# Optimization experiments

Hardware: AMD Instinct MI355X
Metric: run time of the kernel (lower is better)

## Reference

```python
import jax, jax.numpy as jnp
import numpy as np

N = 100000
E = 1600000
NFEAT = 256
NHID = 64
NHEADS = 4
NCLASS = 32
ALPHA = 0.2  # LeakyReLU negative slope


def _xavier_normal(key, shape, gain=1.414):
    fan_in, fan_out = shape[-2], shape[-1]
    std = gain * np.sqrt(2.0 / (fan_in + fan_out))
    return (jax.random.normal(key, shape, jnp.float32) * std).astype(jnp.float32)


def setup_inputs() -> dict:
    key = jax.random.key(0)
    k = jax.random.split(key, 8)
    x = jax.random.normal(k[0], (N, NFEAT), jnp.float32)
    src = jax.random.randint(k[1], (E,), 0, N, jnp.int32)
    dst = jax.random.randint(k[2], (E,), 0, N, jnp.int32)
    # self-loops on the first N edges so every row has nonzero attention mass
    loop = jnp.arange(N, dtype=jnp.int32)
    src = src.at[:N].set(loop)
    dst = dst.at[:N].set(loop)
    edge_index = jnp.stack([src, dst])  # [2, E]
    W_heads = _xavier_normal(k[3], (NHEADS, NFEAT, NHID))
    # torch inits a as (1, 2*out): xavier fans are (2*out, 1)
    a_std = 1.414 * np.sqrt(2.0 / (2 * NHID + 1))
    a_heads = (jax.random.normal(k[4], (NHEADS, 2 * NHID), jnp.float32) * a_std)
    W_out = _xavier_normal(k[5], (NHEADS * NHID, NCLASS))
    a_out_std = 1.414 * np.sqrt(2.0 / (2 * NCLASS + 1))
    a_out = (jax.random.normal(k[6], (2 * NCLASS,), jnp.float32) * a_out_std)
    return {"x": x, "edge_index": edge_index, "W_heads": W_heads,
            "a_heads": a_heads, "W_out": W_out, "a_out": a_out}


def _gat_layer(x, W, a, src, dst):
    """One sparse GAT attention layer (dropout = identity, eval mode)."""
    h = x @ W                      # [N, O]
    O = W.shape[1]
    s_src = h @ a[:O]              # [N]
    s_dst = h @ a[O:]              # [N]
    # e_ij = exp(-leakyrelu(a . [h_i ; h_j])) for edge (i=src, j=dst)
    e = jnp.exp(-jax.nn.leaky_relu(s_src[src] + s_dst[dst], ALPHA))  # [E]
    rowsum = jax.ops.segment_sum(e, src, num_segments=N)             # [N]
    agg = jax.ops.segment_sum(e[:, None] * h[dst], src, num_segments=N)  # [N, O]
    return agg / rowsum[:, None]


def reference(x, edge_index, W_heads, a_heads, W_out, a_out):
    src, dst = edge_index[0], edge_index[1]
    # multi-head hidden layer (concat=True -> elu per head)
    heads = jax.vmap(lambda W, a: _gat_layer(x, W, a, src, dst))(W_heads, a_heads)  # [H, N, NHID]
    x1 = jax.nn.elu(heads).transpose(1, 0, 2).reshape(N, NHEADS * NHID)
    # output attention layer (concat=False), then elu + log_softmax in SpGAT.forward
    h2 = _gat_layer(x1, W_out, a_out, src, dst)  # [N, NCLASS]
    return jax.nn.log_softmax(jax.nn.elu(h2), axis=1)
```

## Files before the change

kernel.cpp:

```cpp
#include <hip/hip_runtime.h>
#include <cstdint>
#include <cstddef>

#define ALPHA 0.2f

__device__ __forceinline__ float lrelu(float x) { return x > 0.f ? x : ALPHA * x; }

__device__ __forceinline__ float qbf(float x)
{
    uint32_t u = __float_as_uint(x);
    uint32_t r = (u + 0x7FFFu + ((u >> 16) & 1u)) & 0xFFFF0000u;
    return __uint_as_float(r);
}

__global__ __launch_bounds__(256) void k_gemm1(const float* __restrict__ x,
                                               const float* __restrict__ Wh,
                                               float* __restrict__ H, int n)
{
    __shared__ float As[32][68];
    __shared__ float Bs[32][256];
    const int tid = threadIdx.x;
    const int row0 = blockIdx.x * 64;
    const int tx = tid & 15, ty = tid >> 4;

    float acc[4][16];
#pragma unroll
    for (int r = 0; r < 4; ++r)
#pragma unroll
        for (int c = 0; c < 16; ++c) acc[r][c] = 0.f;

    for (int k0 = 0; k0 < 256; k0 += 32) {
        for (int j = tid; j < 512; j += 256) {
            int r = j >> 3, kk = (j & 7) << 2;
            int gr = row0 + r; if (gr >= n) gr = n - 1;
            const float4 v = *(const float4*)&x[(size_t)gr * 256 + k0 + kk];
            As[kk + 0][r] = qbf(v.x); As[kk + 1][r] = qbf(v.y);
            As[kk + 2][r] = qbf(v.z); As[kk + 3][r] = qbf(v.w);
        }
        for (int j = tid; j < 2048; j += 256) {
            int kk = j >> 6, c4 = j & 63;
            int h = c4 >> 4, o = (c4 & 15) << 2;
            const float4 v = *(const float4*)&Wh[h * 16384 + (k0 + kk) * 64 + o];
            float* bp = &Bs[kk][c4 << 2];
            bp[0] = qbf(v.x); bp[1] = qbf(v.y); bp[2] = qbf(v.z); bp[3] = qbf(v.w);
        }
        __syncthreads();
#pragma unroll
        for (int kk = 0; kk < 32; ++kk) {
            const float4 a  = *(const float4*)&As[kk][ty << 2];
            const float4 b0 = *(const float4*)&Bs[kk][tx * 16 + 0];
            const float4 b1 = *(const float4*)&Bs[kk][tx * 16 + 4];
            const float4 b2 = *(const float4*)&Bs[kk][tx * 16 + 8];
            const float4 b3 = *(const float4*)&Bs[kk][tx * 16 + 12];
            const float av[4]  = {a.x, a.y, a.z, a.w};
            const float bv[16] = {b0.x, b0.y, b0.z, b0.w, b1.x, b1.y, b1.z, b1.w,
                                  b2.x, b2.y, b2.z, b2.w, b3.x, b3.y, b3.z, b3.w};
#pragma unroll
            for (int r = 0; r < 4; ++r)
#pragma unroll
                for (int c = 0; c < 16; ++c) acc[r][c] += av[r] * bv[c];
        }
        __syncthreads();
    }
#pragma unroll
    for (int r = 0; r < 4; ++r) {
        int gr = row0 + (ty << 2) + r;
        if (gr < n) {
            float* dst = &H[(size_t)gr * 256 + tx * 16];
#pragma unroll
            for (int i = 0; i < 4; ++i)
                *(float4*)&dst[4 * i] = make_float4(acc[r][4 * i + 0], acc[r][4 * i + 1],
                                                    acc[r][4 * i + 2], acc[r][4 * i + 3]);
        }
    }
}

__global__ __launch_bounds__(256) void k_scores1(const float* __restrict__ H,
                                                 const float* __restrict__ a,
                                                 float* __restrict__ s1src,
                                                 float* __restrict__ s1dst, int n)
{
    int gtid = blockIdx.x * 256 + threadIdx.x;
    int node = gtid >> 6, lane = gtid & 63;
    if (node >= n) return;
    int h = lane >> 4, o0 = (lane & 15) << 2;
    const float4 hv = *(const float4*)&H[(size_t)node * 256 + lane * 4];
    float as0 = qbf(a[h * 128 + o0 + 0]), as1 = qbf(a[h * 128 + o0 + 1]);
    float as2 = qbf(a[h * 128 + o0 + 2]), as3 = qbf(a[h * 128 + o0 + 3]);
    float ad0 = qbf(a[h * 128 + 64 + o0 + 0]), ad1 = qbf(a[h * 128 + 64 + o0 + 1]);
    float ad2 = qbf(a[h * 128 + 64 + o0 + 2]), ad3 = qbf(a[h * 128 + 64 + o0 + 3]);
    float ps = hv.x * as0 + hv.y * as1 + hv.z * as2 + hv.w * as3;
    float pd = hv.x * ad0 + hv.y * ad1 + hv.z * ad2 + hv.w * ad3;
#pragma unroll
    for (int m = 8; m >= 1; m >>= 1) {
        ps += __shfl_xor(ps, m);
        pd += __shfl_xor(pd, m);
    }
    if ((lane & 15) == 0) {
        s1src[node * 4 + h] = ps;
        s1dst[node * 4 + h] = pd;
    }
}

__global__ void k_zero(int* __restrict__ p, int n)
{
    int i = blockIdx.x * 256 + threadIdx.x;
    if (i < n) p[i] = 0;
}

__global__ void k_hist(const int* __restrict__ src, int* __restrict__ counts, int e)
{
    int i = blockIdx.x * 256 + threadIdx.x;
    if (i < e) atomicAdd(&counts[src[i]], 1);
}

__global__ __launch_bounds__(256) void k_blocksum(const int* __restrict__ counts,
                                                  int* __restrict__ bsum, int n)
{
    int tid = threadIdx.x;
    int i0 = blockIdx.x * 2048 + tid * 8;
    int s = 0;
#pragma unroll
    for (int k = 0; k < 8; ++k) {
        int i = i0 + k;
        if (i < n) s += counts[i];
    }
#pragma unroll
    for (int m = 32; m >= 1; m >>= 1) s += __shfl_xor(s, m);
    __shared__ int ws[4];
    int lane = tid & 63, wv = tid >> 6;
    if (lane == 0) ws[wv] = s;
    __syncthreads();
    if (tid == 0) bsum[blockIdx.x] = ws[0] + ws[1] + ws[2] + ws[3];
}

__global__ void k_scanmeta(const int* __restrict__ bsum, int* __restrict__ choff, int nchunk)
{
    int lane = threadIdx.x;
    int v = (lane < nchunk) ? bsum[lane] : 0;
    int incl = v;
#pragma unroll
    for (int d = 1; d < 64; d <<= 1) {
        int t = __shfl_up(incl, d);
        if (lane >= d) incl += t;
    }
    if (lane < nchunk) choff[lane] = incl - v;
}

__global__ __launch_bounds__(256) void k_apply(const int* __restrict__ counts,
                                               const int* __restrict__ choff,
                                               int* __restrict__ offsets,
                                               int* __restrict__ cursor, int n)
{
    int tid = threadIdx.x;
    int i0 = blockIdx.x * 2048 + tid * 8;
    int c[8]; int s = 0;
#pragma unroll
    for (int k = 0; k < 8; ++k) {
        int i = i0 + k;
        c[k] = (i < n) ? counts[i] : 0;
        s += c[k];
    }
    int lane = tid & 63, wv = tid >> 6;
    int incl = s;
#pragma unroll
    for (int d = 1; d < 64; d <<= 1) {
        int t = __shfl_up(incl, d);
        if (lane >= d) incl += t;
    }
    __shared__ int ws[4];
    if (lane == 63) ws[wv] = incl;
    __syncthreads();
    int woff = 0;
    for (int w = 0; w < 4; ++w)
        if (w < wv) woff += ws[w];
    int run = incl - s + woff + choff[blockIdx.x];
#pragma unroll
    for (int k = 0; k < 8; ++k) {
        int i = i0 + k;
        if (i < n) { offsets[i] = run; cursor[i] = run; }
        run += c[k];
        if (i == n - 1) offsets[n] = run;
    }
}

__global__ void k_scatter(const int* __restrict__ src,
                          int* __restrict__ cursor, int* __restrict__ csr, int e)
{
    int i = blockIdx.x * 256 + threadIdx.x;
    if (i < e) {
        int pos = atomicAdd(&cursor[src[i]], 1);
        csr[pos] = i;
    }
}

__global__ __launch_bounds__(256) void k_sortcsr(const int* __restrict__ dst_in,
                                                 const int* __restrict__ offsets,
                                                 int* __restrict__ csr, int n)
{
    int gtid = blockIdx.x * 256 + threadIdx.x;
    int node = gtid >> 6, lane = gtid & 63;
    if (node >= n) return;
    int beg = offsets[node], end = offsets[node + 1];
    int cnt = end - beg;
    if (cnt <= 0) return;
    if (cnt <= 64) {
        int v = (lane < cnt) ? csr[beg + lane] : 0x7FFFFFFF;
#pragma unroll
        for (int k = 2; k <= 64; k <<= 1) {
#pragma unroll
            for (int j = k >> 1; j > 0; j >>= 1) {
                int o = __shfl_xor(v, j);
                bool up    = ((lane & k) == 0);
                bool lower = ((lane & j) == 0);
                int mn = min(v, o), mx = max(v, o);
                v = (lower == up) ? mn : mx;
            }
        }
        if (lane < cnt) csr[beg + lane] = dst_in[v];
    } else {
        if (lane == 0) {
            for (int i = beg + 1; i < end; ++i) {
                int key = csr[i]; int j = i - 1;
                while (j >= beg && csr[j] > key) { csr[j + 1] = csr[j]; --j; }
                csr[j + 1] = key;
            }
        }
        __threadfence();
        for (int i = lane; i < cnt; i += 64) {
            int eid = csr[beg + i];
            csr[beg + i] = dst_in[eid];
        }
    }
}

__global__ __launch_bounds__(256) void k_agg1(const int* __restrict__ csr_dst,
                                              const int* __restrict__ offsets,
                                              const float* __restrict__ H,
                                              const float* __restrict__ s1src,
                                              const float* __restrict__ s1dst,
                                              const float* __restrict__ Wout,
                                              const float* __restrict__ aout,
                                              float* __restrict__ h2,
                                              float* __restrict__ s2src,
                                              float* __restrict__ s2dst, int n)
{
    __shared__ float Wt[32][256];
    const int tid = threadIdx.x;
    for (int j = tid; j < 8192; j += 256) {
        int k = j >> 5, c = j & 31;
        Wt[c][k] = qbf(Wout[j]);
    }
    __syncthreads();

    int gtid = blockIdx.x * 256 + tid;
    int node = gtid >> 6, lane = gtid & 63;
    if (node >= n) return;
    int h = lane >> 4;
    int beg = offsets[node], end = offsets[node + 1];
    float ssrc = s1src[node * 4 + h];
    float ax = 0.f, ay = 0.f, az = 0.f, aw = 0.f, wsum = 0.f;
    for (int j = beg; j < end; j += 64) {
        int dvec = (j + lane < end) ? csr_dst[j + lane] : 0;
        int cnt = min(64, end - j);
        for (int t = 0; t < cnt; ++t) {
            int d = __shfl(dvec, t);
            float sd = s1dst[d * 4 + h];
            float w = expf(-lrelu(ssrc + sd));
            const float4 hv = *(const float4*)&H[(size_t)d * 256 + lane * 4];
            ax += w * hv.x; ay += w * hv.y;
            az += w * hv.z; aw += w * hv.w;
            wsum += w;
        }
    }
    float inv = 1.f / wsum;
    float r0 = ax * inv, r1 = ay * inv, r2 = az * inv, r3 = aw * inv;
    r0 = r0 > 0.f ? r0 : expm1f(r0);
    r1 = r1 > 0.f ? r1 : expm1f(r1);
    r2 = r2 > 0.f ? r2 : expm1f(r2);
    r3 = r3 > 0.f ? r3 : expm1f(r3);

    float p[32];
#pragma unroll
    for (int c = 0; c < 32; ++c) {
        const float4 wv = *(const float4*)&Wt[c][lane << 2];
        p[c] = r0 * wv.x + r1 * wv.y + r2 * wv.z + r3 * wv.w;
    }
#pragma unroll
    for (int m = 32; m >= 1; m >>= 1) {
#pragma unroll
        for (int c = 0; c < 32; ++c) p[c] += __shfl_xor(p[c], m);
    }
    if (lane == 0) {
        float ss = 0.f, sd2 = 0.f;
#pragma unroll
        for (int c = 0; c < 32; ++c) {
            ss  += p[c] * qbf(aout[c]);
            sd2 += p[c] * qbf(aout[32 + c]);
        }
        float* dst = &h2[(size_t)node * 32];
#pragma unroll
        for (int i = 0; i < 8; ++i)
            *(float4*)&dst[4 * i] = make_float4(p[4 * i + 0], p[4 * i + 1],
                                                p[4 * i + 2], p[4 * i + 3]);
        s2src[node] = ss;
        s2dst[node] = sd2;
    }
}

__global__ __launch_bounds__(256) void k_agg2(const int* __restrict__ csr_dst,
                                              const int* __restrict__ offsets,
                                              const float* __restrict__ h2,
                                              const float* __restrict__ s2src,
                                              const float* __restrict__ s2dst,
                                              float* __restrict__ out, int n)
{
    int gtid = blockIdx.x * 256 + threadIdx.x;
    int node = gtid >> 6, lane = gtid & 63;
    if (node >= n) return;
    int c = lane & 31;
    int beg = offsets[node], end = offsets[node + 1];
    float ssrc = s2src[node];
    float acc = 0.f, wsum = 0.f;
    for (int j = beg; j < end; j += 64) {
        int dvec = (j + lane < end) ? csr_dst[j + lane] : 0;
        int cnt = min(64, end - j);
        for (int t = 0; t < cnt; ++t) {
            int d = __shfl(dvec, t);
            float sd = s2dst[d];
            float w = expf(-lrelu(ssrc + sd));
            acc += w * h2[(size_t)d * 32 + c];
            wsum += w;
        }
    }
    float v = acc / wsum;
    v = v > 0.f ? v : expm1f(v);
    float m = v;
#pragma unroll
    for (int i = 16; i >= 1; i >>= 1) m = fmaxf(m, __shfl_xor(m, i));
    float ex = expf(v - m);
    float se = ex;
#pragma unroll
    for (int i = 16; i >= 1; i >>= 1) se += __shfl_xor(se, i);
    float r = v - m - logf(se);
    if (lane < 32) out[(size_t)node * 32 + c] = r;
}

extern "C" void kernel_launch(void* const* d_in, const int* in_sizes, int n_in,
                              void* d_out, int out_size, void* d_ws, size_t ws_size,
                              hipStream_t stream)
{
    const float* x    = (const float*)d_in[0];
    const int*   ei   = (const int*)d_in[1];
    const float* Wh   = (const float*)d_in[2];
    const float* ah   = (const float*)d_in[3];
    const float* Wout = (const float*)d_in[4];
    const float* aout = (const float*)d_in[5];
    float* out = (float*)d_out;

    const int n = in_sizes[0] / 256;
    const int e = in_sizes[1] / 2;
    const int* src = ei;
    const int* dst = ei + e;

    auto align = [](size_t v) { return (v + 255) & ~(size_t)255; };
    char* w = (char*)d_ws;
    float* H      = (float*)w; w += align((size_t)n * 256 * 4);
    float* h2     = (float*)w; w += align((size_t)n * 32 * 4);
    int*   csr    = (int*)w;   w += align((size_t)e * 4);
    float* s1src  = (float*)w; w += align((size_t)n * 4 * 4);
    float* s1dst  = (float*)w; w += align((size_t)n * 4 * 4);
    int*   counts = (int*)w;   w += align((size_t)n * 4);
    int*   offs   = (int*)w;   w += align((size_t)(n + 1) * 4);
    int*   cursor = (int*)w;   w += align((size_t)n * 4);
    float* s2src  = (float*)w; w += align((size_t)n * 4);
    float* s2dst  = (float*)w; w += align((size_t)n * 4);
    int*   bsum   = (int*)w;   w += align(4096);
    int*   choff  = (int*)w;   w += align(4096);

    const int nchunk = (n + 2047) / 2048;
    const int gN256  = (n + 255) / 256;
    const int gWave  = (n + 3) / 4;
    const int gE     = (e + 255) / 256;

    k_gemm1<<<(n + 63) / 64, 256, 0, stream>>>(x, Wh, H, n);
    k_scores1<<<gWave, 256, 0, stream>>>(H, ah, s1src, s1dst, n);

    k_zero<<<gN256, 256, 0, stream>>>(counts, n);
    k_hist<<<gE, 256, 0, stream>>>(src, counts, e);
    k_blocksum<<<nchunk, 256, 0, stream>>>(counts, bsum, n);
    k_scanmeta<<<1, 64, 0, stream>>>(bsum, choff, nchunk);
    k_apply<<<nchunk, 256, 0, stream>>>(counts, choff, offs, cursor, n);
    k_scatter<<<gE, 256, 0, stream>>>(src, cursor, csr, e);
    k_sortcsr<<<gWave, 256, 0, stream>>>(dst, offs, csr, n);

    k_agg1<<<gWave, 256, 0, stream>>>(csr, offs, H, s1src, s1dst,
                                      Wout, aout, h2, s2src, s2dst, n);
    k_agg2<<<gWave, 256, 0, stream>>>(csr, offs, h2, s2src, s2dst, out, n);
}
```

Measured before the change: 1.419 ms.

## Fuse score computation into GEMM and precompute per-edge attention weights

Folds the attention score dot products into the first GEMM epilogue, so the separate scores kernel and its re-read of H go away. Sorting now keeps edge ids, and two new edge-parallel kernels compute the CSR-ordered destination array and exp(-leakyrelu) weights for both layers up front. The aggregation kernels then read precomputed weights instead of gathering scores and evaluating exp per neighbor, and they prefetch the next neighbor's row to overlap gathers. The trade-off is extra launches and extra edge-sized buffers (w1 is 4 floats per edge) that must be written and read back.

```diff
diff --git a/kernel.cpp b/kernel.cpp
--- a/kernel.cpp
+++ b/kernel.cpp
@@ -13,15 +13,32 @@
     return __uint_as_float(r);
 }
 
+__device__ __forceinline__ float readlane_f(float v, int l)
+{
+    return __int_as_float(__builtin_amdgcn_readlane(__float_as_int(v), l));
+}
+
 __global__ __launch_bounds__(256) void k_gemm1(const float* __restrict__ x,
                                                const float* __restrict__ Wh,
-                                               float* __restrict__ H, int n)
+                                               const float* __restrict__ a,
+                                               float* __restrict__ H,
+                                               float* __restrict__ s1src,
+                                               float* __restrict__ s1dst, int n)
 {
     __shared__ float As[32][68];
     __shared__ float Bs[32][256];
+    __shared__ float Pa[64][17];
+    __shared__ float Pb[64][17];
+    __shared__ float avs[256], avd[256];
     const int tid = threadIdx.x;
     const int row0 = blockIdx.x * 64;
     const int tx = tid & 15, ty = tid >> 4;
+
+    {
+        int h = tid >> 6, o = tid & 63;
+        avs[tid] = qbf(a[h * 128 + o]);
+        avd[tid] = qbf(a[h * 128 + 64 + o]);
+    }
 
     float acc[4][16];
 #pragma unroll
@@ -47,12 +64,12 @@
         __syncthreads();
 #pragma unroll
         for (int kk = 0; kk < 32; ++kk) {
-            const float4 a  = *(const float4*)&As[kk][ty << 2];
+            const float4 av4 = *(const float4*)&As[kk][ty << 2];
             const float4 b0 = *(const float4*)&Bs[kk][tx * 16 + 0];
             const float4 b1 = *(const float4*)&Bs[kk][tx * 16 + 4];
             const float4 b2 = *(const float4*)&Bs[kk][tx * 16 + 8];
             const float4 b3 = *(const float4*)&Bs[kk][tx * 16 + 12];
-            const float av[4]  = {a.x, a.y, a.z, a.w};
+            const float av[4]  = {av4.x, av4.y, av4.z, av4.w};
             const float bv[16] = {b0.x, b0.y, b0.z, b0.w, b1.x, b1.y, b1.z, b1.w,
                                   b2.x, b2.y, b2.z, b2.w, b3.x, b3.y, b3.z, b3.w};
 #pragma unroll
@@ -64,7 +81,16 @@
     }
 #pragma unroll
     for (int r = 0; r < 4; ++r) {
-        int gr = row0 + (ty << 2) + r;
+        int row = (ty << 2) + r;
+        int gr = row0 + row;
+        float ps = 0.f, pd = 0.f;
+#pragma unroll
+        for (int c = 0; c < 16; ++c) {
+            ps += acc[r][c] * avs[tx * 16 + c];
+            pd += acc[r][c] * avd[tx * 16 + c];
+        }
+        Pa[row][tx] = ps;
+        Pb[row][tx] = pd;
         if (gr < n) {
             float* dst = &H[(size_t)gr * 256 + tx * 16];
 #pragma unroll
@@ -73,32 +99,16 @@
                                                     acc[r][4 * i + 2], acc[r][4 * i + 3]);
         }
     }
-}
-
-__global__ __launch_bounds__(256) void k_scores1(const float* __restrict__ H,
-                                                 const float* __restrict__ a,
-                                                 float* __restrict__ s1src,
-                                                 float* __restrict__ s1dst, int n)
-{
-    int gtid = blockIdx.x * 256 + threadIdx.x;
-    int node = gtid >> 6, lane = gtid & 63;
-    if (node >= n) return;
-    int h = lane >> 4, o0 = (lane & 15) << 2;
-    const float4 hv = *(const float4*)&H[(size_t)node * 256 + lane * 4];
-    float as0 = qbf(a[h * 128 + o0 + 0]), as1 = qbf(a[h * 128 + o0 + 1]);
-    float as2 = qbf(a[h * 128 + o0 + 2]), as3 = qbf(a[h * 128 + o0 + 3]);
-    float ad0 = qbf(a[h * 128 + 64 + o0 + 0]), ad1 = qbf(a[h * 128 + 64 + o0 + 1]);
-    float ad2 = qbf(a[h * 128 + 64 + o0 + 2]), ad3 = qbf(a[h * 128 + 64 + o0 + 3]);
-    float ps = hv.x * as0 + hv.y * as1 + hv.z * as2 + hv.w * as3;
-    float pd = hv.x * ad0 + hv.y * ad1 + hv.z * ad2 + hv.w * ad3;
-#pragma unroll
-    for (int m = 8; m >= 1; m >>= 1) {
-        ps += __shfl_xor(ps, m);
-        pd += __shfl_xor(pd, m);
-    }
-    if ((lane & 15) == 0) {
-        s1src[node * 4 + h] = ps;
-        s1dst[node * 4 + h] = pd;
+    __syncthreads();
+    for (int o = tid; o < 512; o += 256) {
+        int row = o >> 3, h = (o >> 1) & 3, which = o & 1;
+        const float* P = which ? &Pb[row][0] : &Pa[row][0];
+        float s = P[h * 4 + 0] + P[h * 4 + 1] + P[h * 4 + 2] + P[h * 4 + 3];
+        int gr = row0 + row;
+        if (gr < n) {
+            if (which) s1dst[gr * 4 + h] = s;
+            else       s1src[gr * 4 + h] = s;
+        }
     }
 }
 
@@ -194,8 +204,7 @@
     }
 }
 
-__global__ __launch_bounds__(256) void k_sortcsr(const int* __restrict__ dst_in,
-                                                 const int* __restrict__ offsets,
+__global__ __launch_bounds__(256) void k_sortcsr(const int* __restrict__ offsets,
                                                  int* __restrict__ csr, int n)
 {
     int gtid = blockIdx.x * 256 + threadIdx.x;
@@ -217,7 +226,7 @@
                 v = (lower == up) ? mn : mx;
             }
         }
-        if (lane < cnt) csr[beg + lane] = dst_in[v];
+        if (lane < cnt) csr[beg + lane] = v;
     } else {
         if (lane == 0) {
             for (int i = beg + 1; i < end; ++i) {
@@ -226,19 +235,45 @@
                 csr[j + 1] = key;
             }
         }
-        __threadfence();
-        for (int i = lane; i < cnt; i += 64) {
-            int eid = csr[beg + i];
-            csr[beg + i] = dst_in[eid];
-        }
-    }
-}
-
-__global__ __launch_bounds__(256) void k_agg1(const int* __restrict__ csr_dst,
+    }
+}
+
+__global__ void k_w1(const int* __restrict__ csr_eid,
+                     const int* __restrict__ src, const int* __restrict__ dst,
+                     const float* __restrict__ s1src, const float* __restrict__ s1dst,
+                     int* __restrict__ csrd, float* __restrict__ w1, int e)
+{
+    int i = blockIdx.x * 256 + threadIdx.x;
+    if (i >= e) return;
+    int eid = csr_eid[i];
+    int s = src[eid], d = dst[eid];
+    csrd[i] = d;
+    const float4 aa = *(const float4*)&s1src[(size_t)s * 4];
+    const float4 bb = *(const float4*)&s1dst[(size_t)d * 4];
+    float4 w;
+    w.x = expf(-lrelu(aa.x + bb.x));
+    w.y = expf(-lrelu(aa.y + bb.y));
+    w.z = expf(-lrelu(aa.z + bb.z));
+    w.w = expf(-lrelu(aa.w + bb.w));
+    *(float4*)&w1[(size_t)i * 4] = w;
+}
+
+__global__ void k_w2(const int* __restrict__ csr_eid,
+                     const int* __restrict__ src, const int* __restrict__ dst,
+                     const float* __restrict__ s2src, const float* __restrict__ s2dst,
+                     float* __restrict__ w2, int e)
+{
+    int i = blockIdx.x * 256 + threadIdx.x;
+    if (i >= e) return;
+    int eid = csr_eid[i];
+    float z = s2src[src[eid]] + s2dst[dst[eid]];
+    w2[i] = expf(-lrelu(z));
+}
+
+__global__ __launch_bounds__(256) void k_agg1(const int* __restrict__ csrd,
                                               const int* __restrict__ offsets,
                                               const float* __restrict__ H,
-                                              const float* __restrict__ s1src,
-                                              const float* __restrict__ s1dst,
+                                              const float* __restrict__ w1,
                                               const float* __restrict__ Wout,
                                               const float* __restrict__ aout,
                                               float* __restrict__ h2,
@@ -248,30 +283,37 @@
     __shared__ float Wt[32][256];
     const int tid = threadIdx.x;
     for (int j = tid; j < 8192; j += 256) {
-        int k = j >> 5, c = j & 31;
-        Wt[c][k] = qbf(Wout[j]);
+        int c = j >> 8, k = j & 255;
+        Wt[c][k] = qbf(Wout[k * 32 + c]);
     }
     __syncthreads();
 
     int gtid = blockIdx.x * 256 + tid;
     int node = gtid >> 6, lane = gtid & 63;
     if (node >= n) return;
-    int h = lane >> 4;
-    int beg = offsets[node], end = offsets[node + 1];
-    float ssrc = s1src[node * 4 + h];
+    const int beg = offsets[node], end = offsets[node + 1];
+    const int wsel = lane & 48;
     float ax = 0.f, ay = 0.f, az = 0.f, aw = 0.f, wsum = 0.f;
-    for (int j = beg; j < end; j += 64) {
-        int dvec = (j + lane < end) ? csr_dst[j + lane] : 0;
-        int cnt = min(64, end - j);
-        for (int t = 0; t < cnt; ++t) {
-            int d = __shfl(dvec, t);
-            float sd = s1dst[d * 4 + h];
-            float w = expf(-lrelu(ssrc + sd));
-            const float4 hv = *(const float4*)&H[(size_t)d * 256 + lane * 4];
-            ax += w * hv.x; ay += w * hv.y;
-            az += w * hv.z; aw += w * hv.w;
+    for (int j = beg; j < end; j += 16) {
+        int slot = j + (lane & 15);
+        bool okl = slot < end;
+        int dv   = okl ? csrd[slot] : 0;
+        float wv = okl ? w1[(size_t)slot * 4 + (lane >> 4)] : 0.f;
+        int cnt = min(16, end - j);
+        int d = __builtin_amdgcn_readlane(dv, 0);
+        float4 hv = *(const float4*)&H[(size_t)d * 256 + lane * 4];
+        int t = 0;
+        for (; t + 1 < cnt; ++t) {
+            int d2 = __builtin_amdgcn_readlane(dv, t + 1);
+            float4 hv2 = *(const float4*)&H[(size_t)d2 * 256 + lane * 4];
+            float w = __shfl(wv, wsel + t);
+            ax += w * hv.x; ay += w * hv.y; az += w * hv.z; aw += w * hv.w;
             wsum += w;
-        }
+            hv = hv2;
+        }
+        float w = __shfl(wv, wsel + t);
+        ax += w * hv.x; ay += w * hv.y; az += w * hv.z; aw += w * hv.w;
+        wsum += w;
     }
     float inv = 1.f / wsum;
     float r0 = ax * inv, r1 = ay * inv, r2 = az * inv, r3 = aw * inv;
@@ -283,8 +325,8 @@
     float p[32];
 #pragma unroll
     for (int c = 0; c < 32; ++c) {
-        const float4 wv = *(const float4*)&Wt[c][lane << 2];
-        p[c] = r0 * wv.x + r1 * wv.y + r2 * wv.z + r3 * wv.w;
+        const float4 wv4 = *(const float4*)&Wt[c][lane << 2];
+        p[c] = r0 * wv4.x + r1 * wv4.y + r2 * wv4.z + r3 * wv4.w;
     }
 #pragma unroll
     for (int m = 32; m >= 1; m >>= 1) {
@@ -308,11 +350,10 @@
     }
 }
 
-__global__ __launch_bounds__(256) void k_agg2(const int* __restrict__ csr_dst,
+__global__ __launch_bounds__(256) void k_agg2(const int* __restrict__ csrd,
                                               const int* __restrict__ offsets,
                                               const float* __restrict__ h2,
-                                              const float* __restrict__ s2src,
-                                              const float* __restrict__ s2dst,
+                                              const float* __restrict__ w2,
                                               float* __restrict__ out, int n)
 {
     int gtid = blockIdx.x * 256 + threadIdx.x;
@@ -320,18 +361,25 @@
     if (node >= n) return;
     int c = lane & 31;
     int beg = offsets[node], end = offsets[node + 1];
-    float ssrc = s2src[node];
     float acc = 0.f, wsum = 0.f;
     for (int j = beg; j < end; j += 64) {
-        int dvec = (j + lane < end) ? csr_dst[j + lane] : 0;
+        int slot = j + lane;
+        bool okl = slot < end;
+        int dv    = okl ? csrd[slot] : 0;
+        float wvv = okl ? w2[slot] : 0.f;
         int cnt = min(64, end - j);
-        for (int t = 0; t < cnt; ++t) {
-            int d = __shfl(dvec, t);
-            float sd = s2dst[d];
-            float w = expf(-lrelu(ssrc + sd));
-            acc += w * h2[(size_t)d * 32 + c];
-            wsum += w;
-        }
+        int d = __builtin_amdgcn_readlane(dv, 0);
+        float hv = h2[(size_t)d * 32 + c];
+        int t = 0;
+        for (; t + 1 < cnt; ++t) {
+            int d2 = __builtin_amdgcn_readlane(dv, t + 1);
+            float hv2 = h2[(size_t)d2 * 32 + c];
+            float w = readlane_f(wvv, t);
+            acc += w * hv; wsum += w;
+            hv = hv2;
+        }
+        float w = readlane_f(wvv, t);
+        acc += w * hv; wsum += w;
     }
     float v = acc / wsum;
     v = v > 0.f ? v : expm1f(v);
@@ -368,6 +416,9 @@
     float* H      = (float*)w; w += align((size_t)n * 256 * 4);
     float* h2     = (float*)w; w += align((size_t)n * 32 * 4);
     int*   csr    = (int*)w;   w += align((size_t)e * 4);
+    int*   csrd   = (int*)w;   w += align((size_t)e * 4);
+    float* w1     = (float*)w; w += align((size_t)e * 4 * 4);
+    float* w2     = (float*)w; w += align((size_t)e * 4);
     float* s1src  = (float*)w; w += align((size_t)n * 4 * 4);
     float* s1dst  = (float*)w; w += align((size_t)n * 4 * 4);
     int*   counts = (int*)w;   w += align((size_t)n * 4);
@@ -383,8 +434,7 @@
     const int gWave  = (n + 3) / 4;
     const int gE     = (e + 255) / 256;
 
-    k_gemm1<<<(n + 63) / 64, 256, 0, stream>>>(x, Wh, H, n);
-    k_scores1<<<gWave, 256, 0, stream>>>(H, ah, s1src, s1dst, n);
+    k_gemm1<<<(n + 63) / 64, 256, 0, stream>>>(x, Wh, ah, H, s1src, s1dst, n);
 
     k_zero<<<gN256, 256, 0, stream>>>(counts, n);
     k_hist<<<gE, 256, 0, stream>>>(src, counts, e);
@@ -392,9 +442,13 @@
     k_scanmeta<<<1, 64, 0, stream>>>(bsum, choff, nchunk);
     k_apply<<<nchunk, 256, 0, stream>>>(counts, choff, offs, cursor, n);
     k_scatter<<<gE, 256, 0, stream>>>(src, cursor, csr, e);
-    k_sortcsr<<<gWave, 256, 0, stream>>>(dst, offs, csr, n);
-
-    k_agg1<<<gWave, 256, 0, stream>>>(csr, offs, H, s1src, s1dst,
-                                      Wout, aout, h2, s2src, s2dst, n);
-    k_agg2<<<gWave, 256, 0, stream>>>(csr, offs, h2, s2src, s2dst, out, n);
-}
+    k_sortcsr<<<gWave, 256, 0, stream>>>(offs, csr, n);
+
+    k_w1<<<gE, 256, 0, stream>>>(csr, src, dst, s1src, s1dst, csrd, w1, e);
+
+    k_agg1<<<gWave, 256, 0, stream>>>(csrd, offs, H, w1, Wout, aout,
+                                      h2, s2src, s2dst, n);
+    k_w2<<<gE, 256, 0, stream>>>(csr, src, dst, s2src, s2dst, w2, e);
+
+    k_agg2<<<gWave, 256, 0, stream>>>(csrd, offs, h2, w2, out, n);
+}
```

Measured after the change: 1.311 ms. 7.7% less time.
